# Optimization experiments

Measured on AMD Instinct MI355X. Metric: run time of the kernel, lower is better.

The kernel has to match this reference:

```python
import jax, jax.numpy as jnp
import numpy as np

N_NETWORKS = 4
BETA = 2.0          # CustomHopfield beta = 2.0
UPDATE_STEPS = 4    # update_steps_max=4 fixed-point iterations


def setup_inputs() -> dict:
    key = jax.random.key(0)
    k0, k1, k2, k3 = jax.random.split(key, 4)
    B, IN_DIM, E = 256, 784, 128          # batch hardcoded by repeat(256,...)
    N_EMB = 32768                          # stored patterns per network
    return {
        "x": jax.random.normal(k0, (B, IN_DIM), jnp.float32),
        # embeddings: [n_networks * n_emb, E + 1]; last column is dropped (keys = emb[..., :-1])
        "embeddings": jax.random.normal(k1, (N_NETWORKS * N_EMB, E + 1), jnp.float32),
        "W_enc": jax.random.normal(k2, (IN_DIM, E), jnp.float32) / np.float32(np.sqrt(IN_DIM)),
        "b_enc": jnp.zeros((E,), jnp.float32),
        "W_lin": jax.random.normal(k3, (E * N_NETWORKS, 10), jnp.float32) / np.float32(np.sqrt(E * N_NETWORKS)),
        "b_lin": jnp.zeros((10,), jnp.float32),
    }


def reference(x, embeddings, W_enc, b_enc, W_lin, b_lin):
    B = x.shape[0]
    E = W_enc.shape[1]
    # keys per Hopfield network: [N, K, E] (identity projections: input_size=1, num_heads=1)
    keys = embeddings[:, :-1].reshape(N_NETWORKS, -1, E)
    z = x @ W_enc + b_enc                                   # encoder -> [B, E]
    q = jnp.broadcast_to(z[None], (N_NETWORKS, B, E))       # each network queries same z
    for _ in range(UPDATE_STEPS):
        # modern continuous Hopfield update: q <- softmax(beta * q K^T) K
        attn = jax.nn.softmax(BETA * jnp.einsum('nbe,nke->nbk', q, keys), axis=-1)
        q = jnp.einsum('nbk,nke->nbe', attn, keys)
    z_cat = jnp.transpose(q, (1, 0, 2)).reshape(B, N_NETWORKS * E)  # concat per-network retrievals
    return jax.nn.log_softmax(jax.nn.relu(z_cat) @ W_lin + b_lin, axis=-1)
```

## Files before the change

### kernel.cpp

```cpp
#include <hip/hip_runtime.h>
#include <hip/hip_bf16.h>
#include <cstdint>
#include <cstddef>


#define NNET 4
#define NQ   256
#define EDIM 128
#define NKEY 32768
#define ESTR 129
#define QT   32
#define NCHUNK 32
#define KPC  (NKEY/NCHUNK)
#define KQ   256
#define SCAN_WAVES 4
#define KPW  (KPC/SCAN_WAVES)
#define SLICES (KPW/16)
#define SROW (QT/16)
#define BLOCKCAP 64
#define SURV_CAP 512
#define WCAP 1024
#define MITCAP 128
#define EMIT_MARGIN 10.0f
#define SEL_MARGIN  9.5f
#define REL_MARGIN  9.75f

typedef _Float16 half8 __attribute__((ext_vector_type(8)));
typedef float f32x4v __attribute__((ext_vector_type(4)));

__device__ __forceinline__ float dec16(unsigned v) {
  _Float16 h = __builtin_bit_cast(_Float16, (unsigned short)(v & 0xFFFFu));
  return (float)h;
}
__device__ __forceinline__ unsigned pack16(int key, float s) {
  unsigned short hb = __builtin_bit_cast(unsigned short, (_Float16)s);
  return ((unsigned)key << 16) | (unsigned)hb;
}
__device__ __forceinline__ unsigned enc_f32(float f) {
  unsigned u = __float_as_uint(f);
  return (u & 0x80000000u) ? ~u : (u | 0x80000000u);
}
__device__ __forceinline__ float dec_f32(unsigned e) {
  unsigned u = (e & 0x80000000u) ? (e & 0x7FFFFFFFu) : ~e;
  return __uint_as_float(u);
}

__global__ __launch_bounds__(128)
void enc_kernel(const float* __restrict__ x, const float* __restrict__ We,
                const float* __restrict__ be, float* __restrict__ q0,
                int* __restrict__ gw) {
  const int b = blockIdx.x, tid = threadIdx.x;
  __shared__ float xs[784];
  for (int i = tid; i < 784; i += 128) xs[i] = x[b * 784 + i];
  __syncthreads();
  float acc = be[tid];
  for (int i = 0; i < 784; ++i) acc += xs[i] * We[i * EDIM + tid];
#pragma unroll
  for (int n = 0; n < NNET; ++n) q0[((size_t)n * NQ + b) * EDIM + tid] = acc;
  if (b == 0 && tid < 4) gw[tid] = 0;
}

typedef _Float16 half4v __attribute__((ext_vector_type(4)));
__global__ __launch_bounds__(256)
void keyprep_kernel(const float* __restrict__ emb, _Float16* __restrict__ kh) {
  const size_t quads = (size_t)NNET * NKEY * EDIM / 4;
  for (size_t i4 = (size_t)blockIdx.x * 256 + threadIdx.x; i4 < quads;
       i4 += (size_t)gridDim.x * 256) {
    const size_t row = i4 >> 5;
    const int col = (int)(i4 & 31) * 4;
    const float* src = emb + row * ESTR + col;
    half4v h;
#pragma unroll
    for (int j = 0; j < 4; ++j) h[j] = (_Float16)src[j];
    *(half4v*)(kh + i4 * 4) = h;
  }
}

template <bool F16K>
__global__ __launch_bounds__(SCAN_WAVES * 64)
void scan_kernel(const float* __restrict__ qcur, const float* __restrict__ emb,
                 const _Float16* __restrict__ keysh,
                 int* __restrict__ cntb, float* __restrict__ cmaxb,
                 unsigned* __restrict__ cand,
                 int* __restrict__ gw, int* __restrict__ wit) {
  const int wg = blockIdx.x;
  const int window = wg >> 6;
  const int within = wg & 63;
  const int xcd = within & 7;
  const int qt = within >> 3;
  const int c = window * 8 + xcd;
  const int net = c >> 5, chunk = c & 31;

  const int tid = threadIdx.x;
  const int lane = tid & 63;
  const int g = lane >> 4, ln = lane & 15;

  __shared__ unsigned lmax[QT];
  __shared__ int lcnt[QT];
  __shared__ unsigned lbuf[QT][BLOCKCAP];
  if (tid < QT) { lmax[tid] = enc_f32(-3.4e38f); lcnt[tid] = 0; }

  half8 aq[SROW][4];
  {
    const float* qb = qcur + ((size_t)net * NQ + qt * QT) * EDIM;
#pragma unroll
    for (int s = 0; s < SROW; ++s)
#pragma unroll
      for (int f = 0; f < 4; ++f) {
        const float* p = qb + (s * 16 + ln) * EDIM + f * 32 + g * 8;
        half8 h;
#pragma unroll
        for (int j = 0; j < 8; ++j) h[j] = (_Float16)(2.0f * p[j]);
        aq[s][f] = h;
      }
  }
  __syncthreads();

  const int w = tid >> 6;
  const int key0 = chunk * KPC + w * KPW;

  auto loadPair = [&](int p, half8 buf[2][4]) {
#pragma unroll
    for (int u = 0; u < 2; ++u) {
      const int sl = 2 * p + u;
      const size_t keyrow = (size_t)net * NKEY + key0 + sl * 16 + ln;
      if constexpr (F16K) {
        const _Float16* kp = keysh + keyrow * EDIM + g * 8;
#pragma unroll
        for (int f = 0; f < 4; ++f) buf[u][f] = *(const half8*)(kp + f * 32);
      } else {
        const float* kp = emb + keyrow * ESTR + g * 8;
#pragma unroll
        for (int f = 0; f < 4; ++f) {
          half8 h;
#pragma unroll
          for (int j = 0; j < 8; ++j) h[j] = (_Float16)kp[f * 32 + j];
          buf[u][f] = h;
        }
      }
    }
  };

  float rowmax[SROW * 4];
#pragma unroll
  for (int i = 0; i < SROW * 4; ++i) rowmax[i] = -3.4e38f;

  half8 bA[2][4], bB[2][4];
  loadPair(0, bA);

#pragma unroll
  for (int grp = 0; grp < SLICES / 4; ++grp) {
    loadPair(2 * grp + 1, bB);

    f32x4v acc[4][SROW];
#pragma unroll
    for (int u = 0; u < 4; ++u)
#pragma unroll
      for (int s = 0; s < SROW; ++s) acc[u][s] = f32x4v{0.f, 0.f, 0.f, 0.f};

#pragma unroll
    for (int u = 0; u < 2; ++u)
#pragma unroll
      for (int f = 0; f < 4; ++f)
#pragma unroll
        for (int s = 0; s < SROW; ++s)
          acc[u][s] = __builtin_amdgcn_mfma_f32_16x16x32_f16(aq[s][f], bA[u][f], acc[u][s], 0, 0, 0);

    if (grp < SLICES / 4 - 1) loadPair(2 * grp + 2, bA);

#pragma unroll
    for (int u = 0; u < 2; ++u)
#pragma unroll
      for (int f = 0; f < 4; ++f)
#pragma unroll
        for (int s = 0; s < SROW; ++s)
          acc[u + 2][s] = __builtin_amdgcn_mfma_f32_16x16x32_f16(aq[s][f], bB[u][f], acc[u + 2][s], 0, 0, 0);

#pragma unroll
    for (int u = 0; u < 4; ++u)
#pragma unroll
      for (int s = 0; s < SROW; ++s)
#pragma unroll
        for (int r = 0; r < 4; ++r)
          rowmax[s * 4 + r] = fmaxf(rowmax[s * 4 + r], acc[u][s][r]);
#pragma unroll
    for (int d = 1; d < 16; d <<= 1)
#pragma unroll
      for (int i = 0; i < SROW * 4; ++i)
        rowmax[i] = fmaxf(rowmax[i], __shfl_xor(rowmax[i], d, 64));

#pragma unroll
    for (int u = 0; u < 4; ++u) {
      const int keyg = key0 + (grp * 4 + u) * 16 + ln;
#pragma unroll
      for (int s = 0; s < SROW; ++s)
#pragma unroll
        for (int r = 0; r < 4; ++r)
          if (acc[u][s][r] >= rowmax[s * 4 + r] - EMIT_MARGIN) {
            const int q = s * 16 + g * 4 + r;
            const int slot = atomicAdd(&lcnt[q], 1);
            if (slot < BLOCKCAP) lbuf[q][slot] = pack16(keyg, acc[u][s][r]);
          }
    }
  }

  if (ln == 0) {
#pragma unroll
    for (int i = 0; i < SROW * 4; ++i)
      atomicMax(&lmax[(i >> 2) * 16 + g * 4 + (i & 3)], enc_f32(rowmax[i]));
  }
  __syncthreads();

  const size_t qbase = (size_t)net * NQ + qt * QT;
  for (int j = tid; j < QT * BLOCKCAP; j += SCAN_WAVES * 64) {
    const int q = j >> 6, i = j & (BLOCKCAP - 1);
    const int cq = lcnt[q];
    if (i < (cq < BLOCKCAP ? cq : BLOCKCAP))
      cand[((qbase + q) * NCHUNK + chunk) * BLOCKCAP + i] = lbuf[q][i];
  }
  if (tid < QT) {
    const size_t cell = (qbase + tid) * NCHUNK + chunk;
    cntb[cell] = lcnt[tid];
    cmaxb[cell] = dec_f32(lmax[tid]);
    if (lcnt[tid] > BLOCKCAP) {
      int i = atomicAdd(gw, 4);
#pragma unroll
      for (int qq = 0; qq < 4; ++qq)
        if (i + qq < WCAP) wit[i + qq] = ((int)cell << 2) | qq;
    }
  }
}

__global__ __launch_bounds__(256)
void dense_kernel(const float* __restrict__ qcur, const float* __restrict__ emb,
                  const int* __restrict__ gw, const int* __restrict__ wit,
                  float* __restrict__ pm, float* __restrict__ pl,
                  float* __restrict__ po) {
  const int tid = threadIdx.x, lane = tid & 63, w = tid >> 6;
  const int grp = lane >> 3;
  const int le = lane & 7;
  int nwork = *gw;
  if (nwork > WCAP) nwork = WCAP;

  __shared__ float qv[EDIM];
  __shared__ float sc[KQ];
  __shared__ int klist[KQ];
  __shared__ float osh[EDIM];
  __shared__ float red[8];
  __shared__ int nsig;

  for (int it = blockIdx.x; it < nwork; it += gridDim.x) {
    const int v = wit[it];
    const int slot = v >> 7;
    const int chunk = (v >> 2) & 31;
    const int qq = v & 3;
    const int net = slot >> 8;
    const int kbase = chunk * KPC + qq * KQ;

    if (tid < EDIM) qv[tid] = 2.0f * qcur[(size_t)slot * EDIM + tid];
    if (tid == 0) nsig = 0;
    __syncthreads();

    const float* base = emb + ((size_t)net * NKEY + kbase) * ESTR;
    for (int pp = 0; pp < 8; pp += 4) {
      float s[4] = {0.f, 0.f, 0.f, 0.f};
      const float* kr[4];
#pragma unroll
      for (int u = 0; u < 4; ++u)
        kr[u] = base + (size_t)(w * 64 + (pp + u) * 8 + grp) * ESTR + le;
#pragma unroll
      for (int i = 0; i < 16; ++i) {
        const float qe = qv[le + 8 * i];
#pragma unroll
        for (int u = 0; u < 4; ++u) s[u] += qe * kr[u][8 * i];
      }
#pragma unroll
      for (int d = 1; d < 8; d <<= 1)
#pragma unroll
        for (int u = 0; u < 4; ++u) s[u] += __shfl_xor(s[u], d, 64);
      if (le == 0) {
#pragma unroll
        for (int u = 0; u < 4; ++u) sc[w * 64 + (pp + u) * 8 + grp] = s[u];
      }
    }
    __syncthreads();

    float m = sc[tid];
#pragma unroll
    for (int d = 32; d; d >>= 1) m = fmaxf(m, __shfl_xor(m, d, 64));
    if (lane == 0) red[w] = m;
    __syncthreads();
    const float m_c = fmaxf(fmaxf(red[0], red[1]), fmaxf(red[2], red[3]));

    const float ev = expf(sc[tid] - m_c);
    sc[tid] = ev;
    float l = ev;
#pragma unroll
    for (int d = 32; d; d >>= 1) l += __shfl_xor(l, d, 64);
    if (lane == 0) red[4 + w] = l;
    if (ev > 1e-9f) {
      const int pos = atomicAdd(&nsig, 1);
      klist[pos] = tid;
    }
    __syncthreads();
    const float l_c = red[4] + red[5] + red[6] + red[7];
    const int msig = nsig;

    const int e = tid & 127, hf = tid >> 7;
    float acc = 0.f;
    for (int j = hf; j < msig; j += 2) {
      const int kk = klist[j];
      acc += sc[kk] * emb[((size_t)net * NKEY + kbase + kk) * ESTR + e];
    }
    if (hf) osh[e] = acc;
    __syncthreads();
    if (!hf) po[(size_t)it * EDIM + e] = acc + osh[e];
    if (tid == 0) { pm[it] = m_c; pl[it] = l_c; }
    __syncthreads();
  }
}

__global__ __launch_bounds__(256)
void refine_kernel(const float* __restrict__ qcur, const float* __restrict__ emb,
                   const int* __restrict__ cntb, const float* __restrict__ cmaxb,
                   const unsigned* __restrict__ cand, float* __restrict__ qnext,
                   const int* __restrict__ gw, const int* __restrict__ wit,
                   const float* __restrict__ pm, const float* __restrict__ pl,
                   const float* __restrict__ po) {
  const int q = blockIdx.x, net = blockIdx.y;
  const int tid = threadIdx.x, lane = tid & 63, w = tid >> 6;
  const int slot = net * NQ + q;
  __shared__ float qv[EDIM];
  __shared__ float osh[EDIM];
  __shared__ int ccnt[NCHUNK];
  __shared__ float cmax[NCHUNK];
  __shared__ int keys[SURV_CAP];
  __shared__ float exsc[SURV_CAP];
  __shared__ int mit[MITCAP];
  __shared__ int nmit;
  __shared__ int nsurv;
  __shared__ float gmax_s;
  __shared__ float red[8];

  int nwork = *gw;
  if (nwork > WCAP) nwork = WCAP;

  if (tid < EDIM) qv[tid] = 2.0f * qcur[(size_t)slot * EDIM + tid];
  if (tid < NCHUNK) {
    ccnt[tid] = cntb[(size_t)slot * NCHUNK + tid];
    cmax[tid] = cmaxb[(size_t)slot * NCHUNK + tid];
  }
  if (tid == 0) { nsurv = 0; nmit = 0; }
  __syncthreads();
  if (tid == 0) {
    float gv = -3.4e38f;
    for (int c = 0; c < NCHUNK; ++c) gv = fmaxf(gv, cmax[c]);
    gmax_s = gv;
  }
  for (int it = tid; it < nwork; it += 256) {
    if ((wit[it] >> 7) == slot) {
      const int i = atomicAdd(&nmit, 1);
      if (i < MITCAP) mit[i] = it;
    }
  }
  __syncthreads();
  const float G = gmax_s;
  const int nm = nmit < MITCAP ? nmit : MITCAP;

  for (int j = tid; j < NCHUNK * BLOCKCAP; j += 256) {
    const int c = j >> 6, i = j & (BLOCKCAP - 1);
    if (cmax[c] < G - REL_MARGIN) continue;
    const int cc = ccnt[c];
    if (cc > BLOCKCAP) continue;
    if (i < cc) {
      const unsigned pv = cand[((size_t)slot * NCHUNK + c) * BLOCKCAP + i];
      if (dec16(pv) >= G - SEL_MARGIN) {
        const int k = atomicAdd(&nsurv, 1);
        if (k < SURV_CAP) keys[k] = (int)(pv >> 16);
      }
    }
  }
  __syncthreads();
  int m = nsurv < SURV_CAP ? nsurv : SURV_CAP;

  for (int j = w; j < m; j += 4) {
    const float* kr = emb + ((size_t)net * NKEY + keys[j]) * ESTR;
    float p2 = qv[2 * lane] * kr[2 * lane] + qv[2 * lane + 1] * kr[2 * lane + 1];
#pragma unroll
    for (int d = 32; d; d >>= 1) p2 += __shfl_xor(p2, d, 64);
    if (lane == 0) exsc[j] = p2;
  }
  __syncthreads();
  if (w == 0) {
    float em = -3.4e38f;
    for (int j = lane; j < m; j += 64) em = fmaxf(em, exsc[j]);
#pragma unroll
    for (int d = 32; d; d >>= 1) em = fmaxf(em, __shfl_xor(em, d, 64));
    if (lane == 0) red[0] = em;
  }
  __syncthreads();
  const float em = red[0];
  for (int j = tid; j < m; j += 256) exsc[j] = expf(exsc[j] - em);
  __syncthreads();
  if (w == 0) {
    float l = 0.f;
    for (int j = lane; j < m; j += 64) l += exsc[j];
#pragma unroll
    for (int d = 32; d; d >>= 1) l += __shfl_xor(l, d, 64);
    if (lane == 0) red[1] = l;
  }
  __syncthreads();

  if (tid == 0) {
    float mstar = (m > 0) ? em : -3.4e38f;
    for (int j = 0; j < nm; ++j) mstar = fmaxf(mstar, pm[mit[j]]);
    float ltot = (m > 0) ? red[1] * expf(em - mstar) : 0.f;
    for (int j = 0; j < nm; ++j) ltot += pl[mit[j]] * expf(pm[mit[j]] - mstar);
    red[2] = mstar;
    red[3] = ltot;
  }
  __syncthreads();
  const float mstar = red[2];
  const float inv = 1.0f / red[3];

  const int e = tid & 127, hf = tid >> 7;
  float acc = 0.f;
  for (int j = hf; j < m; j += 2)
    acc += exsc[j] * emb[((size_t)net * NKEY + keys[j]) * ESTR + e];
  if (hf) osh[e] = acc;
  __syncthreads();
  if (!hf) {
    float o = (m > 0) ? (acc + osh[e]) * expf(em - mstar) : 0.f;
    for (int j = 0; j < nm; ++j)
      o += po[(size_t)mit[j] * EDIM + e] * expf(pm[mit[j]] - mstar);
    qnext[(size_t)slot * EDIM + e] = o * inv;
  }
}

__global__ __launch_bounds__(64)
void head_kernel(const float* __restrict__ qf, const float* __restrict__ Wl,
                 const float* __restrict__ bl, float* __restrict__ out) {
  const int b = blockIdx.x, lane = threadIdx.x;
  float acc[10];
#pragma unroll
  for (int c = 0; c < 10; ++c) acc[c] = 0.f;
  for (int t = lane; t < NNET * EDIM; t += 64) {
    float z = qf[((size_t)(t >> 7) * NQ + b) * EDIM + (t & 127)];
    z = fmaxf(z, 0.f);
    const float* wr = Wl + t * 10;
#pragma unroll
    for (int c = 0; c < 10; ++c) acc[c] += z * wr[c];
  }
#pragma unroll
  for (int d = 32; d; d >>= 1)
#pragma unroll
    for (int c = 0; c < 10; ++c) acc[c] += __shfl_xor(acc[c], d, 64);
  if (lane == 0) {
    float lg[10], mxv = -3.4e38f;
#pragma unroll
    for (int c = 0; c < 10; ++c) {
      lg[c] = acc[c] + bl[c];
      mxv = fmaxf(mxv, lg[c]);
    }
    float s = 0.f;
#pragma unroll
    for (int c = 0; c < 10; ++c) s += expf(lg[c] - mxv);
    float lse = mxv + logf(s);
#pragma unroll
    for (int c = 0; c < 10; ++c) out[b * 10 + c] = lg[c] - lse;
  }
}

extern "C" void kernel_launch(void* const* d_in, const int* in_sizes, int n_in,
                              void* d_out, int out_size, void* d_ws, size_t ws_size,
                              hipStream_t stream) {
  (void)in_sizes; (void)n_in; (void)out_size;
  const float* x   = (const float*)d_in[0];
  const float* emb = (const float*)d_in[1];
  const float* We  = (const float*)d_in[2];
  const float* be  = (const float*)d_in[3];
  const float* Wl  = (const float*)d_in[4];
  const float* bl  = (const float*)d_in[5];
  float* out = (float*)d_out;

  char* p = (char*)d_ws;
  float* q0 = (float*)p;    p += (size_t)NNET * NQ * EDIM * 4;
  float* q1 = (float*)p;    p += (size_t)NNET * NQ * EDIM * 4;
  int* cntb = (int*)p;      p += (size_t)NNET * NQ * NCHUNK * 4;
  float* cmaxb = (float*)p; p += (size_t)NNET * NQ * NCHUNK * 4;
  unsigned* cand = (unsigned*)p; p += (size_t)NNET * NQ * NCHUNK * BLOCKCAP * 4;
  int* gw = (int*)p;        p += 16;
  int* wit = (int*)p;       p += (size_t)4 * WCAP * 4;
  float* pm = (float*)p;    p += (size_t)WCAP * 4;
  float* pl = (float*)p;    p += (size_t)WCAP * 4;
  float* po = (float*)p;    p += (size_t)WCAP * EDIM * 4;
  _Float16* kh = (_Float16*)p;
  const bool f16k =
      ((size_t)(p - (char*)d_ws) + (size_t)NNET * NKEY * EDIM * 2) <= ws_size;

  enc_kernel<<<dim3(NQ), dim3(128), 0, stream>>>(x, We, be, q0, gw);
  if (f16k)
    keyprep_kernel<<<dim3(4096), dim3(256), 0, stream>>>(emb, kh);

  const int nblocks = NNET * NCHUNK * (NQ / QT);
  float* qa = q0;
  float* qb = q1;
  for (int step = 0; step < 4; ++step) {
    int* gws = gw + step;
    int* wits = wit + step * WCAP;
    if (f16k)
      scan_kernel<true><<<dim3(nblocks), dim3(SCAN_WAVES * 64), 0, stream>>>(
          qa, emb, kh, cntb, cmaxb, cand, gws, wits);
    else
      scan_kernel<false><<<dim3(nblocks), dim3(SCAN_WAVES * 64), 0, stream>>>(
          qa, emb, (const _Float16*)nullptr, cntb, cmaxb, cand, gws, wits);
    dense_kernel<<<dim3(256), dim3(256), 0, stream>>>(qa, emb, gws, wits, pm, pl, po);
    refine_kernel<<<dim3(NQ, NNET), dim3(256), 0, stream>>>(
        qa, emb, cntb, cmaxb, cand, qb, gws, wits, pm, pl, po);
    float* t = qa; qa = qb; qb = t;
  }
  head_kernel<<<dim3(NQ), dim3(64), 0, stream>>>(qa, Wl, bl, out);
}
```

Before: 293.9 us.

## Double query tile per scan block and use rotating four-slice key prefetch

Raises the query tile per scan workgroup from 32 to 64 rows, so each key slice loaded from memory feeds twice as many MFMA row blocks and the block count per window halves. The block-index decode is updated for the new tile count. The key prefetch is restructured from paired double buffers into a four-slice ring, processing two slices per step and refilling each buffer right after use. Risks are higher register pressure from larger query fragments and accumulators, lower occupancy, and that other kernels relying on QT (shared buffers, grid size) must stay consistent.

Measured after the change: 339.3 us. 15.5% more time.

```diff
diff --git a/kernel.cpp b/kernel.cpp
--- a/kernel.cpp
+++ b/kernel.cpp
@@ -9,7 +9,7 @@
 #define EDIM 128
 #define NKEY 32768
 #define ESTR 129
-#define QT   32
+#define QT   64
 #define NCHUNK 32
 #define KPC  (NKEY/NCHUNK)
 #define KQ   256
@@ -84,10 +84,9 @@
                  unsigned* __restrict__ cand,
                  int* __restrict__ gw, int* __restrict__ wit) {
   const int wg = blockIdx.x;
-  const int window = wg >> 6;
-  const int within = wg & 63;
-  const int xcd = within & 7;
-  const int qt = within >> 3;
+  const int xcd = wg & 7;
+  const int qt = (wg >> 3) & 3;
+  const int window = wg >> 5;
   const int c = window * 8 + xcd;
   const int net = c >> 5, chunk = c & 31;
 
@@ -118,25 +117,22 @@
 
   const int w = tid >> 6;
   const int key0 = chunk * KPC + w * KPW;
-
-  auto loadPair = [&](int p, half8 buf[2][4]) {
-#pragma unroll
-    for (int u = 0; u < 2; ++u) {
-      const int sl = 2 * p + u;
-      const size_t keyrow = (size_t)net * NKEY + key0 + sl * 16 + ln;
-      if constexpr (F16K) {
-        const _Float16* kp = keysh + keyrow * EDIM + g * 8;
-#pragma unroll
-        for (int f = 0; f < 4; ++f) buf[u][f] = *(const half8*)(kp + f * 32);
-      } else {
-        const float* kp = emb + keyrow * ESTR + g * 8;
-#pragma unroll
-        for (int f = 0; f < 4; ++f) {
-          half8 h;
-#pragma unroll
-          for (int j = 0; j < 8; ++j) h[j] = (_Float16)kp[f * 32 + j];
-          buf[u][f] = h;
-        }
+  const _Float16* kwb = F16K ? (keysh + ((size_t)net * NKEY + key0) * EDIM) : nullptr;
+  const float* ewb = emb + ((size_t)net * NKEY + key0) * ESTR;
+
+  auto loadSlice = [&](int sl, half8 buf[4]) {
+    if constexpr (F16K) {
+      const _Float16* kp = kwb + (sl * 16 + ln) * EDIM + g * 8;
+#pragma unroll
+      for (int f = 0; f < 4; ++f) buf[f] = *(const half8*)(kp + f * 32);
+    } else {
+      const float* kp = ewb + (sl * 16 + ln) * ESTR + g * 8;
+#pragma unroll
+      for (int f = 0; f < 4; ++f) {
+        half8 h;
+#pragma unroll
+        for (int j = 0; j < 8; ++j) h[j] = (_Float16)kp[f * 32 + j];
+        buf[f] = h;
       }
     }
   };
@@ -145,39 +141,37 @@
 #pragma unroll
   for (int i = 0; i < SROW * 4; ++i) rowmax[i] = -3.4e38f;
 
-  half8 bA[2][4], bB[2][4];
-  loadPair(0, bA);
-
-#pragma unroll
-  for (int grp = 0; grp < SLICES / 4; ++grp) {
-    loadPair(2 * grp + 1, bB);
-
-    f32x4v acc[4][SROW];
-#pragma unroll
-    for (int u = 0; u < 4; ++u)
+  half8 b[4][4];
+  loadSlice(0, b[0]);
+  loadSlice(1, b[1]);
+  loadSlice(2, b[2]);
+  loadSlice(3, b[3]);
+
+#pragma unroll
+  for (int pp = 0; pp < SLICES / 2; ++pp) {
+    const int s0 = 2 * pp, s1 = 2 * pp + 1;
+    f32x4v acc[2][SROW];
+#pragma unroll
+    for (int u = 0; u < 2; ++u)
 #pragma unroll
       for (int s = 0; s < SROW; ++s) acc[u][s] = f32x4v{0.f, 0.f, 0.f, 0.f};
 
 #pragma unroll
+    for (int f = 0; f < 4; ++f)
+#pragma unroll
+      for (int s = 0; s < SROW; ++s)
+        acc[0][s] = __builtin_amdgcn_mfma_f32_16x16x32_f16(aq[s][f], b[s0 & 3][f], acc[0][s], 0, 0, 0);
+    if (s0 + 4 < SLICES) loadSlice(s0 + 4, b[s0 & 3]);
+
+#pragma unroll
+    for (int f = 0; f < 4; ++f)
+#pragma unroll
+      for (int s = 0; s < SROW; ++s)
+        acc[1][s] = __builtin_amdgcn_mfma_f32_16x16x32_f16(aq[s][f], b[s1 & 3][f], acc[1][s], 0, 0, 0);
+    if (s1 + 4 < SLICES) loadSlice(s1 + 4, b[s1 & 3]);
+
+#pragma unroll
     for (int u = 0; u < 2; ++u)
-#pragma unroll
-      for (int f = 0; f < 4; ++f)
-#pragma unroll
-        for (int s = 0; s < SROW; ++s)
-          acc[u][s] = __builtin_amdgcn_mfma_f32_16x16x32_f16(aq[s][f], bA[u][f], acc[u][s], 0, 0, 0);
-
-    if (grp < SLICES / 4 - 1) loadPair(2 * grp + 2, bA);
-
-#pragma unroll
-    for (int u = 0; u < 2; ++u)
-#pragma unroll
-      for (int f = 0; f < 4; ++f)
-#pragma unroll
-        for (int s = 0; s < SROW; ++s)
-          acc[u + 2][s] = __builtin_amdgcn_mfma_f32_16x16x32_f16(aq[s][f], bB[u][f], acc[u + 2][s], 0, 0, 0);
-
-#pragma unroll
-    for (int u = 0; u < 4; ++u)
 #pragma unroll
       for (int s = 0; s < SROW; ++s)
 #pragma unroll
@@ -190,8 +184,8 @@
         rowmax[i] = fmaxf(rowmax[i], __shfl_xor(rowmax[i], d, 64));
 
 #pragma unroll
-    for (int u = 0; u < 4; ++u) {
-      const int keyg = key0 + (grp * 4 + u) * 16 + ln;
+    for (int u = 0; u < 2; ++u) {
+      const int keyg = key0 + (2 * pp + u) * 16 + ln;
 #pragma unroll
       for (int s = 0; s < SROW; ++s)
 #pragma unroll
```
